# Performance work log

Hardware: AMD Instinct MI355X
Metric: run time of the kernel (lower is better)

## Reference

```python
import jax, jax.numpy as jnp
import numpy as np

B, S, D = 4, 2048, 1024
H = 16
DK = D // H  # 64

def setup_inputs() -> dict:
    key = jax.random.key(0)
    ks = jax.random.split(key, 5)
    scale = 0.02
    return {
        "x": jax.random.normal(ks[0], (B, S, D), dtype=jnp.float32),
        "Wq": jax.random.normal(ks[1], (D, D), dtype=jnp.float32) * scale,
        "Wk": jax.random.normal(ks[2], (D, D), dtype=jnp.float32) * scale,
        "Wv": jax.random.normal(ks[3], (D, D), dtype=jnp.float32) * scale,
        "Wo": jax.random.normal(ks[4], (D, D), dtype=jnp.float32) * scale,
    }

def reference(x, Wq, Wk, Wv, Wo):
    b, s, d = x.shape
    h, dk = H, DK
    # torch nn.Linear(bias=False): y = x @ W.T
    q = (x @ Wq.T).reshape(b, s, h, dk).transpose(0, 2, 1, 3)  # [b,h,s,dk]
    k = (x @ Wk.T).reshape(b, s, h, dk).transpose(0, 2, 1, 3)
    v = (x @ Wv.T).reshape(b, s, h, dk).transpose(0, 2, 1, 3)
    scores = jnp.einsum('bhqd,bhkd->bhqk', q, k) * (dk ** -0.5)
    causal = jnp.triu(jnp.ones((s, s), dtype=bool), k=1)  # True = masked out
    scores = jnp.where(causal, -jnp.inf, scores)
    probs = jax.nn.softmax(scores, axis=-1)
    attn = jnp.einsum('bhqk,bhkd->bhqd', probs, v)  # [b,h,s,dk]
    attn = attn.transpose(0, 2, 1, 3).reshape(b, s, d)
    return attn @ Wo.T
```

## Files before the change

### kernel.cpp

```cpp
#include <hip/hip_runtime.h>

typedef __attribute__((ext_vector_type(8))) short bf16x8;
typedef __attribute__((ext_vector_type(4))) float f32x4;
typedef unsigned int u32;
typedef unsigned short u16;

constexpr int Bb = 4, S = 2048, D = 1024, H = 16, DK = 64, M = Bb * S;

#if __has_builtin(__builtin_amdgcn_exp2f)
#define EXP2F __builtin_amdgcn_exp2f
#else
#define EXP2F exp2f
#endif

__device__ __forceinline__ u16 f2bf(float f) {
  u32 u = __float_as_uint(f);
  return (u16)((u + 0x7fffu + ((u >> 16) & 1u)) >> 16);
}

__device__ __forceinline__ void gld_lds16(const u16* g, u16* l) {
  __builtin_amdgcn_global_load_lds((const __attribute__((address_space(1))) u32*)g,
                                   (__attribute__((address_space(3))) u32*)l, 16, 0, 0);
}

__global__ void cast_kernel(const float* __restrict__ s, u16* __restrict__ d, int n) {
  int i = (blockIdx.x * blockDim.x + threadIdx.x) * 4;
  if (i >= n) return;
  float4 f = *(const float4*)(s + i);
  ushort4 o;
  o.x = f2bf(f.x); o.y = f2bf(f.y); o.z = f2bf(f.z); o.w = f2bf(f.w);
  *(ushort4*)(d + i) = o;
}

struct CastArgs { const float* s[4]; u16* d[4]; float sc[4]; };
__global__ void cast4_kernel(CastArgs a) {
  int i = (blockIdx.x * blockDim.x + threadIdx.x) * 4;
  int w = i >> 20;
  int off = i & ((1 << 20) - 1);
  float sc = a.sc[w];
  float4 f = *(const float4*)(a.s[w] + off);
  ushort4 o;
  o.x = f2bf(f.x * sc); o.y = f2bf(f.y * sc); o.z = f2bf(f.z * sc); o.w = f2bf(f.w * sc);
  *(ushort4*)(a.d[w] + off) = o;
}

template <bool OUTF32>
__device__ __forceinline__ void gemm_core(const u16* __restrict__ A,
                                          const u16* __restrict__ Bt,
                                          float* __restrict__ Cf, u16* __restrict__ Cb,
                                          int Nn, int Kk, int m0, int n0,
                                          u16* As, u16* Bs) {
  const int tid = threadIdx.x, wave = tid >> 6, lane = tid & 63;
  const int quad = lane >> 4, col = lane & 15;
  const int wm = wave >> 1, wn = wave & 1;

  f32x4 acc[4][4];
#pragma unroll
  for (int i = 0; i < 4; i++)
#pragma unroll
    for (int j = 0; j < 4; j++) acc[i][j] = (f32x4){0.f, 0.f, 0.f, 0.f};

  for (int k0 = 0; k0 < Kk; k0 += 64) {
#pragma unroll
    for (int j = 0; j < 4; j++) {
      int g = (wave * 4 + j) * 64;
      int gl = g + lane;
      int r = gl >> 3, sl = gl & 7;
      int kof = (sl ^ (r & 7)) * 8;
      const u16* ga = A + (size_t)(m0 + r) * Kk + k0 + kof;
      gld_lds16(ga, &As[g * 8]);
      const u16* gb = Bt + (size_t)(n0 + r) * Kk + k0 + kof;
      gld_lds16(gb, &Bs[g * 8]);
    }
    __syncthreads();
#pragma unroll
    for (int kb = 0; kb < 2; kb++) {
      bf16x8 af[4], bfr[4];
#pragma unroll
      for (int mi = 0; mi < 4; mi++) {
        int R = wm * 64 + mi * 16 + col;
        af[mi] = *(const bf16x8*)&As[R * 64 + (((kb * 4 + quad) ^ (R & 7)) << 3)];
      }
#pragma unroll
      for (int ni = 0; ni < 4; ni++) {
        int R = wn * 64 + ni * 16 + col;
        bfr[ni] = *(const bf16x8*)&Bs[R * 64 + (((kb * 4 + quad) ^ (R & 7)) << 3)];
      }
#pragma unroll
      for (int mi = 0; mi < 4; mi++)
#pragma unroll
        for (int ni = 0; ni < 4; ni++)
          acc[mi][ni] = __builtin_amdgcn_mfma_f32_16x16x32_bf16(af[mi], bfr[ni], acc[mi][ni], 0, 0, 0);
    }
    __syncthreads();
  }
#pragma unroll
  for (int mi = 0; mi < 4; mi++)
#pragma unroll
    for (int ni = 0; ni < 4; ni++)
#pragma unroll
      for (int r = 0; r < 4; r++) {
        int row = m0 + wm * 64 + mi * 16 + quad * 4 + r;
        int cc = n0 + wn * 64 + ni * 16 + col;
        float v = acc[mi][ni][r];
        if (OUTF32) Cf[(size_t)row * Nn + cc] = v;
        else Cb[(size_t)row * Nn + cc] = f2bf(v);
      }
}

struct QkvArgs { const u16* bt[3]; u16* c[3]; };
__global__ __launch_bounds__(256) void gemm_qkv(const u16* __restrict__ A, QkvArgs q) {
  __shared__ __align__(16) u16 As[128 * 64];
  __shared__ __align__(16) u16 Bs[128 * 64];
  int sel = blockIdx.x >> 3;
  int n0 = (blockIdx.x & 7) * 128, m0 = blockIdx.y * 128;
  gemm_core<false>(A, q.bt[sel], nullptr, q.c[sel], D, D, m0, n0, As, Bs);
}

__global__ __launch_bounds__(256) void gemm_f32(const u16* __restrict__ A,
                                                const u16* __restrict__ Bt,
                                                float* __restrict__ C) {
  __shared__ __align__(16) u16 As[128 * 64];
  __shared__ __align__(16) u16 Bs[128 * 64];
  gemm_core<true>(A, Bt, C, nullptr, D, D, blockIdx.y * 128, blockIdx.x * 128, As, Bs);
}

__global__ __launch_bounds__(256) void attn_kernel(const u16* __restrict__ Q,
                                                   const u16* __restrict__ K,
                                                   const u16* __restrict__ V,
                                                   u16* __restrict__ O) {
  __shared__ __align__(16) u16 Ks[2][2][64 * 32];
  __shared__ __align__(16) u16 Vt[2][64 * 64];
  __shared__ __align__(16) u16 Pw[4][16 * 64];
  const int tid = threadIdx.x, wave = tid >> 6, lane = tid & 63;
  const int quad = lane >> 4, col = lane & 15;
  const int bh = blockIdx.x, b = bh >> 4, h = bh & 15;
  const int ya = blockIdx.y & 3, yk = blockIdx.y >> 2;
  const int qb = (yk == 0) ? ya : (yk == 1) ? 7 - ya : (yk == 2) ? 8 + ya : 15 - ya;
  const size_t base = (size_t)b * S * D + h * DK;
  const int qw = qb * 128 + wave * 32;
  const int nkt = 2 * qb + 2;

  bf16x8 aq[2][2];
#pragma unroll
  for (int mi = 0; mi < 2; mi++)
#pragma unroll
    for (int kb = 0; kb < 2; kb++)
      aq[mi][kb] = *(const bf16x8*)(Q + base + (size_t)(qw + mi * 16 + col) * D + kb * 32 + quad * 8);

  f32x4 ao[2][4], lacc[2];
#pragma unroll
  for (int mi = 0; mi < 2; mi++) {
    lacc[mi] = (f32x4){0.f, 0.f, 0.f, 0.f};
#pragma unroll
    for (int dg = 0; dg < 4; dg++) ao[mi][dg] = (f32x4){0.f, 0.f, 0.f, 0.f};
  }
  bf16x8 bones;
#pragma unroll
  for (int e = 0; e < 8; e++) bones[e] = (short)0x3F80;

  const int vk0 = (tid & 31) * 2;
  const int vdg = tid >> 5;

  bf16x8 vA0, vA1, vB0, vB1;
  {
    const u16* vp = V + base + (size_t)vk0 * D + vdg * 8;
    vA0 = *(const bf16x8*)vp; vA1 = *(const bf16x8*)(vp + D);
  }
  {
    int c = tid, cb = wave * 64;
    const u16* g0 = K + base + (size_t)(c >> 2) * D + (c & 3) * 8;
    gld_lds16(g0, &Ks[0][0][cb * 8]);
    gld_lds16(g0 + 32, &Ks[0][1][cb * 8]);
  }
  auto vstage = [&](int buf, bf16x8 r0, bf16x8 r1) {
    int kgrp = vk0 >> 3, kin = vk0 & 7;
    int perm = (kgrp ^ vdg) & 7;
#pragma unroll
    for (int e = 0; e < 8; e++) {
      u32 val = ((u32)(u16)r0[e]) | ((u32)(u16)r1[e] << 16);
      *(u32*)&Vt[buf][(vdg * 8 + e) * 64 + perm * 8 + kin] = val;
    }
  };
  vstage(0, vA0, vA1);
  {
    const u16* vp = V + base + (size_t)(64 + vk0) * D + vdg * 8;
    vB0 = *(const bf16x8*)vp; vB1 = *(const bf16x8*)(vp + D);
  }

  for (int kt = 0; kt < nkt; kt++) {
    const int bf = kt & 1, nb = bf ^ 1;
    __syncthreads();
    const bool active = (kt * 64 <= qw + 31);
    if (kt + 1 < nkt) {
      {
        int c = tid, cb = wave * 64;
        const u16* g0 = K + base + (size_t)((kt + 1) * 64 + (c >> 2)) * D + (c & 3) * 8;
        gld_lds16(g0, &Ks[nb][0][cb * 8]);
        gld_lds16(g0 + 32, &Ks[nb][1][cb * 8]);
      }
      vstage(nb, bf ? vA0 : vB0, bf ? vA1 : vB1);
      if (kt + 2 < nkt) {
        const u16* vp = V + base + (size_t)((kt + 2) * 64 + vk0) * D + vdg * 8;
        if (bf) { vB0 = *(const bf16x8*)vp; vB1 = *(const bf16x8*)(vp + D); }
        else    { vA0 = *(const bf16x8*)vp; vA1 = *(const bf16x8*)(vp + D); }
      }
    }
    if (!active) continue;
    f32x4 sacc[2][4];
#pragma unroll
    for (int mi = 0; mi < 2; mi++)
#pragma unroll
      for (int n16 = 0; n16 < 4; n16++) sacc[mi][n16] = (f32x4){0.f, 0.f, 0.f, 0.f};
    {
      bf16x8 bk0[4], bk1[4];
#pragma unroll
      for (int n16 = 0; n16 < 4; n16++) {
        bk0[n16] = *(const bf16x8*)&Ks[bf][0][(n16 * 16 + col) * 32 + quad * 8];
        bk1[n16] = *(const bf16x8*)&Ks[bf][1][(n16 * 16 + col) * 32 + quad * 8];
      }
#pragma unroll
      for (int mi = 0; mi < 2; mi++)
#pragma unroll
        for (int n16 = 0; n16 < 4; n16++) {
          sacc[mi][n16] = __builtin_amdgcn_mfma_f32_16x16x32_bf16(aq[mi][0], bk0[n16], sacc[mi][n16], 0, 0, 0);
          sacc[mi][n16] = __builtin_amdgcn_mfma_f32_16x16x32_bf16(aq[mi][1], bk1[n16], sacc[mi][n16], 0, 0, 0);
        }
    }
    const bool full = (kt * 64 + 63) <= qw;
    bf16x8 bv[2][4];
#pragma unroll
    for (int kb = 0; kb < 2; kb++)
#pragma unroll
      for (int dg = 0; dg < 4; dg++) {
        int d3 = (dg * 2 + (col >> 3)) & 7;
        bv[kb][dg] = *(const bf16x8*)&Vt[bf][(dg * 16 + col) * 64 + (((kb * 4 + quad) ^ d3) << 3)];
      }
#pragma unroll
    for (int mi = 0; mi < 2; mi++) {
#pragma unroll
      for (int r = 0; r < 4; r++) {
        int row16 = quad * 4 + r;
        int qs = quad << 1;
#pragma unroll
        for (int n16 = 0; n16 < 4; n16++) {
          float p = EXP2F(sacc[mi][n16][r]);
          if (!full) {
            int kg = kt * 64 + n16 * 16 + col;
            p = (kg > qw + mi * 16 + row16) ? 0.f : p;
          }
          int kgl = n16 * 16 + col;
          int perm = ((kgl >> 3) ^ qs) & 7;
          Pw[wave][row16 * 64 + perm * 8 + (kgl & 7)] = (u16)(__float_as_uint(p) >> 16);
        }
      }
      int qs2 = ((col >> 2) & 3) << 1;
      bf16x8 ap0 = *(const bf16x8*)&Pw[wave][col * 64 + (((quad ^ qs2) & 7) << 3)];
      bf16x8 ap1 = *(const bf16x8*)&Pw[wave][col * 64 + ((((4 + quad) ^ qs2) & 7) << 3)];
#pragma unroll
      for (int dg = 0; dg < 4; dg++) {
        ao[mi][dg] = __builtin_amdgcn_mfma_f32_16x16x32_bf16(ap0, bv[0][dg], ao[mi][dg], 0, 0, 0);
        ao[mi][dg] = __builtin_amdgcn_mfma_f32_16x16x32_bf16(ap1, bv[1][dg], ao[mi][dg], 0, 0, 0);
      }
      lacc[mi] = __builtin_amdgcn_mfma_f32_16x16x32_bf16(ap0, bones, lacc[mi], 0, 0, 0);
      lacc[mi] = __builtin_amdgcn_mfma_f32_16x16x32_bf16(ap1, bones, lacc[mi], 0, 0, 0);
    }
  }
#pragma unroll
  for (int mi = 0; mi < 2; mi++)
#pragma unroll
    for (int r = 0; r < 4; r++) {
      float inv = 1.f / lacc[mi][r];
      int q = qw + mi * 16 + quad * 4 + r;
#pragma unroll
      for (int dg = 0; dg < 4; dg++)
        O[base + (size_t)q * D + dg * 16 + col] = f2bf(ao[mi][dg][r] * inv);
    }
}

extern "C" void kernel_launch(void* const* d_in, const int* in_sizes, int n_in,
                              void* d_out, int out_size, void* d_ws, size_t ws_size,
                              hipStream_t stream) {
  const float* x  = (const float*)d_in[0];
  const float* Wq = (const float*)d_in[1];
  const float* Wk = (const float*)d_in[2];
  const float* Wv = (const float*)d_in[3];
  const float* Wo = (const float*)d_in[4];

  u16* xb  = (u16*)d_ws;
  u16* wqb = xb + (size_t)M * D;
  u16* wkb = wqb + (size_t)D * D;
  u16* wvb = wkb + (size_t)D * D;
  u16* wob = wvb + (size_t)D * D;
  u16* Qb  = wob + (size_t)D * D;
  u16* Kb  = Qb + (size_t)M * D;
  u16* Vb  = Kb + (size_t)M * D;
  u16* Ab  = xb;

  cast_kernel<<<M * D / 1024, 256, 0, stream>>>(x, xb, M * D);
  CastArgs ca;
  ca.s[0] = Wq; ca.s[1] = Wk; ca.s[2] = Wv; ca.s[3] = Wo;
  ca.d[0] = wqb; ca.d[1] = wkb; ca.d[2] = wvb; ca.d[3] = wob;
  ca.sc[0] = 0.18033688011112042f;
  ca.sc[1] = 1.f; ca.sc[2] = 1.f; ca.sc[3] = 1.f;
  cast4_kernel<<<4 * D * D / 1024, 256, 0, stream>>>(ca);

  QkvArgs qa;
  qa.bt[0] = wqb; qa.bt[1] = wkb; qa.bt[2] = wvb;
  qa.c[0] = Qb; qa.c[1] = Kb; qa.c[2] = Vb;
  gemm_qkv<<<dim3(24, M / 128), 256, 0, stream>>>(xb, qa);

  attn_kernel<<<dim3(Bb * H, 16), 256, 0, stream>>>(Qb, Kb, Vb, Ab);

  gemm_f32<<<dim3(D / 128, M / 128), 256, 0, stream>>>(Ab, wob, (float*)d_out);
}
```

Before: 281.1 us.

## Split long causal query blocks across two workgroups and merge partials in a norm pass

Each workgroup pair now handles a heavy query block (15-p) and a light one (p). The heavy block's key range is split at tile 17 between the two workgroups, and the light block is appended to the second. The split blocks write unnormalized bf16 partial outputs and row sums into scratch space in the output buffer, and a new norm kernel adds and normalizes them. The goal is to balance causal work across workgroups and remove the tail of long blocks, at the cost of an extra launch, scratch traffic, and bf16 rounding of the partials before the merge.

```diff
diff --git a/kernel.cpp b/kernel.cpp
--- a/kernel.cpp
+++ b/kernel.cpp
@@ -16,6 +16,9 @@
 __device__ __forceinline__ u16 f2bf(float f) {
   u32 u = __float_as_uint(f);
   return (u16)((u + 0x7fffu + ((u >> 16) & 1u)) >> 16);
+}
+__device__ __forceinline__ float bf2f(u16 x) {
+  return __uint_as_float(((u32)x) << 16);
 }
 
 __device__ __forceinline__ void gld_lds16(const u16* g, u16* l) {
@@ -128,33 +131,28 @@
 __global__ __launch_bounds__(256) void attn_kernel(const u16* __restrict__ Q,
                                                    const u16* __restrict__ K,
                                                    const u16* __restrict__ V,
-                                                   u16* __restrict__ O) {
+                                                   u16* __restrict__ O,
+                                                   u16* __restrict__ Po,
+                                                   float* __restrict__ Lf) {
   __shared__ __align__(16) u16 Ks[2][2][64 * 32];
   __shared__ __align__(16) u16 Vt[2][64 * 64];
   __shared__ __align__(16) u16 Pw[4][16 * 64];
   const int tid = threadIdx.x, wave = tid >> 6, lane = tid & 63;
   const int quad = lane >> 4, col = lane & 15;
   const int bh = blockIdx.x, b = bh >> 4, h = bh & 15;
-  const int ya = blockIdx.y & 3, yk = blockIdx.y >> 2;
-  const int qb = (yk == 0) ? ya : (yk == 1) ? 7 - ya : (yk == 2) ? 8 + ya : 15 - ya;
+  const int j = blockIdx.y, p = j >> 1, role = j & 1;
+  const int qbh = 15 - p, Th = 2 * qbh + 2;
   const size_t base = (size_t)b * S * D + h * DK;
-  const int qw = qb * 128 + wave * 32;
-  const int nkt = 2 * qb + 2;
-
-  bf16x8 aq[2][2];
-#pragma unroll
-  for (int mi = 0; mi < 2; mi++)
-#pragma unroll
-    for (int kb = 0; kb < 2; kb++)
-      aq[mi][kb] = *(const bf16x8*)(Q + base + (size_t)(qw + mi * 16 + col) * D + kb * 32 + quad * 8);
-
-  f32x4 ao[2][4], lacc[2];
-#pragma unroll
-  for (int mi = 0; mi < 2; mi++) {
-    lacc[mi] = (f32x4){0.f, 0.f, 0.f, 0.f};
-#pragma unroll
-    for (int dg = 0; dg < 4; dg++) ao[mi][dg] = (f32x4){0.f, 0.f, 0.f, 0.f};
+
+  int segQb[2], segK0[2], segK1[2], nseg;
+  if (role == 0) {
+    nseg = 1; segQb[0] = qbh; segK0[0] = 0; segK1[0] = 17;
+  } else {
+    nseg = 2;
+    segQb[0] = qbh; segK0[0] = 17; segK1[0] = Th;
+    segQb[1] = p;   segK0[1] = 0;  segK1[1] = 2 * p + 2;
   }
+
   bf16x8 bones;
 #pragma unroll
   for (int e = 0; e < 8; e++) bones[e] = (short)0x3F80;
@@ -162,120 +160,179 @@
   const int vk0 = (tid & 31) * 2;
   const int vdg = tid >> 5;
 
-  bf16x8 vA0, vA1, vB0, vB1;
-  {
-    const u16* vp = V + base + (size_t)vk0 * D + vdg * 8;
-    vA0 = *(const bf16x8*)vp; vA1 = *(const bf16x8*)(vp + D);
+  for (int s = 0; s < nseg; s++) {
+    const int sqb = segQb[s], k0s = segK0[s], k1s = segK1[s];
+    const int qw = sqb * 128 + wave * 32;
+    const bool partial = (sqb >= 8);
+
+    bf16x8 aq[2][2];
+#pragma unroll
+    for (int mi = 0; mi < 2; mi++)
+#pragma unroll
+      for (int kb = 0; kb < 2; kb++)
+        aq[mi][kb] = *(const bf16x8*)(Q + base + (size_t)(qw + mi * 16 + col) * D + kb * 32 + quad * 8);
+
+    f32x4 ao[2][4], lacc[2];
+#pragma unroll
+    for (int mi = 0; mi < 2; mi++) {
+      lacc[mi] = (f32x4){0.f, 0.f, 0.f, 0.f};
+#pragma unroll
+      for (int dg = 0; dg < 4; dg++) ao[mi][dg] = (f32x4){0.f, 0.f, 0.f, 0.f};
+    }
+
+    bf16x8 vA0, vA1, vB0, vB1;
+    {
+      const u16* vp = V + base + (size_t)(k0s * 64 + vk0) * D + vdg * 8;
+      vA0 = *(const bf16x8*)vp; vA1 = *(const bf16x8*)(vp + D);
+    }
+    __syncthreads();
+    {
+      int c = tid, cb = wave * 64;
+      const u16* g0 = K + base + (size_t)(k0s * 64 + (c >> 2)) * D + (c & 3) * 8;
+      gld_lds16(g0, &Ks[0][0][cb * 8]);
+      gld_lds16(g0 + 32, &Ks[0][1][cb * 8]);
+    }
+    auto vstage = [&](int buf, bf16x8 r0, bf16x8 r1) {
+      int kgrp = vk0 >> 3, kin = vk0 & 7;
+      int perm = (kgrp ^ vdg) & 7;
+#pragma unroll
+      for (int e = 0; e < 8; e++) {
+        u32 val = ((u32)(u16)r0[e]) | ((u32)(u16)r1[e] << 16);
+        *(u32*)&Vt[buf][(vdg * 8 + e) * 64 + perm * 8 + kin] = val;
+      }
+    };
+    vstage(0, vA0, vA1);
+    if (k0s + 1 < k1s) {
+      const u16* vp = V + base + (size_t)((k0s + 1) * 64 + vk0) * D + vdg * 8;
+      vB0 = *(const bf16x8*)vp; vB1 = *(const bf16x8*)(vp + D);
+    }
+
+    for (int kt = k0s; kt < k1s; kt++) {
+      const int ib = (kt - k0s) & 1, nb = ib ^ 1;
+      __syncthreads();
+      const bool active = (kt * 64 <= qw + 31);
+      if (kt + 1 < k1s) {
+        {
+          int c = tid, cb = wave * 64;
+          const u16* g0 = K + base + (size_t)((kt + 1) * 64 + (c >> 2)) * D + (c & 3) * 8;
+          gld_lds16(g0, &Ks[nb][0][cb * 8]);
+          gld_lds16(g0 + 32, &Ks[nb][1][cb * 8]);
+        }
+        vstage(nb, ib ? vA0 : vB0, ib ? vA1 : vB1);
+        if (kt + 2 < k1s) {
+          const u16* vp = V + base + (size_t)((kt + 2) * 64 + vk0) * D + vdg * 8;
+          if (ib) { vB0 = *(const bf16x8*)vp; vB1 = *(const bf16x8*)(vp + D); }
+          else    { vA0 = *(const bf16x8*)vp; vA1 = *(const bf16x8*)(vp + D); }
+        }
+      }
+      if (!active) continue;
+      f32x4 sacc[2][4];
+#pragma unroll
+      for (int mi = 0; mi < 2; mi++)
+#pragma unroll
+        for (int n16 = 0; n16 < 4; n16++) sacc[mi][n16] = (f32x4){0.f, 0.f, 0.f, 0.f};
+      {
+        bf16x8 bk0[4], bk1[4];
+#pragma unroll
+        for (int n16 = 0; n16 < 4; n16++) {
+          bk0[n16] = *(const bf16x8*)&Ks[ib][0][(n16 * 16 + col) * 32 + quad * 8];
+          bk1[n16] = *(const bf16x8*)&Ks[ib][1][(n16 * 16 + col) * 32 + quad * 8];
+        }
+#pragma unroll
+        for (int mi = 0; mi < 2; mi++)
+#pragma unroll
+          for (int n16 = 0; n16 < 4; n16++) {
+            sacc[mi][n16] = __builtin_amdgcn_mfma_f32_16x16x32_bf16(aq[mi][0], bk0[n16], sacc[mi][n16], 0, 0, 0);
+            sacc[mi][n16] = __builtin_amdgcn_mfma_f32_16x16x32_bf16(aq[mi][1], bk1[n16], sacc[mi][n16], 0, 0, 0);
+          }
+      }
+      const bool full = (kt * 64 + 63) <= qw;
+      bf16x8 bv[2][4];
+#pragma unroll
+      for (int kb = 0; kb < 2; kb++)
+#pragma unroll
+        for (int dg = 0; dg < 4; dg++) {
+          int d3 = (dg * 2 + (col >> 3)) & 7;
+          bv[kb][dg] = *(const bf16x8*)&Vt[ib][(dg * 16 + col) * 64 + (((kb * 4 + quad) ^ d3) << 3)];
+        }
+#pragma unroll
+      for (int mi = 0; mi < 2; mi++) {
+#pragma unroll
+        for (int r = 0; r < 4; r++) {
+          int row16 = quad * 4 + r;
+          int qs = quad << 1;
+#pragma unroll
+          for (int n16 = 0; n16 < 4; n16++) {
+            float pv = EXP2F(sacc[mi][n16][r]);
+            if (!full) {
+              int kg = kt * 64 + n16 * 16 + col;
+              pv = (kg > qw + mi * 16 + row16) ? 0.f : pv;
+            }
+            int kgl = n16 * 16 + col;
+            int perm = ((kgl >> 3) ^ qs) & 7;
+            Pw[wave][row16 * 64 + perm * 8 + (kgl & 7)] = (u16)(__float_as_uint(pv) >> 16);
+          }
+        }
+        int qs2 = ((col >> 2) & 3) << 1;
+        bf16x8 ap0 = *(const bf16x8*)&Pw[wave][col * 64 + (((quad ^ qs2) & 7) << 3)];
+        bf16x8 ap1 = *(const bf16x8*)&Pw[wave][col * 64 + ((((4 + quad) ^ qs2) & 7) << 3)];
+#pragma unroll
+        for (int dg = 0; dg < 4; dg++) {
+          ao[mi][dg] = __builtin_amdgcn_mfma_f32_16x16x32_bf16(ap0, bv[0][dg], ao[mi][dg], 0, 0, 0);
+          ao[mi][dg] = __builtin_amdgcn_mfma_f32_16x16x32_bf16(ap1, bv[1][dg], ao[mi][dg], 0, 0, 0);
+        }
+        lacc[mi] = __builtin_amdgcn_mfma_f32_16x16x32_bf16(ap0, bones, lacc[mi], 0, 0, 0);
+        lacc[mi] = __builtin_amdgcn_mfma_f32_16x16x32_bf16(ap1, bones, lacc[mi], 0, 0, 0);
+      }
+    }
+    if (!partial) {
+#pragma unroll
+      for (int mi = 0; mi < 2; mi++)
+#pragma unroll
+        for (int r = 0; r < 4; r++) {
+          float inv = 1.f / lacc[mi][r];
+          int q = qw + mi * 16 + quad * 4 + r;
+#pragma unroll
+          for (int dg = 0; dg < 4; dg++)
+            O[base + (size_t)q * D + dg * 16 + col] = f2bf(ao[mi][dg][r] * inv);
+        }
+    } else {
+      int slot = role * 512 + bh * 8 + p;
+      u16* po = Po + (size_t)slot * 8192;
+      float* lf = Lf + slot * 128;
+#pragma unroll
+      for (int mi = 0; mi < 2; mi++)
+#pragma unroll
+        for (int r = 0; r < 4; r++) {
+          int row = wave * 32 + mi * 16 + quad * 4 + r;
+#pragma unroll
+          for (int dg = 0; dg < 4; dg++)
+            po[row * 64 + dg * 16 + col] = f2bf(ao[mi][dg][r]);
+          if (col == 0) lf[row] = lacc[mi][r];
+        }
+    }
   }
-  {
-    int c = tid, cb = wave * 64;
-    const u16* g0 = K + base + (size_t)(c >> 2) * D + (c & 3) * 8;
-    gld_lds16(g0, &Ks[0][0][cb * 8]);
-    gld_lds16(g0 + 32, &Ks[0][1][cb * 8]);
-  }
-  auto vstage = [&](int buf, bf16x8 r0, bf16x8 r1) {
-    int kgrp = vk0 >> 3, kin = vk0 & 7;
-    int perm = (kgrp ^ vdg) & 7;
-#pragma unroll
-    for (int e = 0; e < 8; e++) {
-      u32 val = ((u32)(u16)r0[e]) | ((u32)(u16)r1[e] << 16);
-      *(u32*)&Vt[buf][(vdg * 8 + e) * 64 + perm * 8 + kin] = val;
-    }
-  };
-  vstage(0, vA0, vA1);
-  {
-    const u16* vp = V + base + (size_t)(64 + vk0) * D + vdg * 8;
-    vB0 = *(const bf16x8*)vp; vB1 = *(const bf16x8*)(vp + D);
-  }
-
-  for (int kt = 0; kt < nkt; kt++) {
-    const int bf = kt & 1, nb = bf ^ 1;
-    __syncthreads();
-    const bool active = (kt * 64 <= qw + 31);
-    if (kt + 1 < nkt) {
-      {
-        int c = tid, cb = wave * 64;
-        const u16* g0 = K + base + (size_t)((kt + 1) * 64 + (c >> 2)) * D + (c & 3) * 8;
-        gld_lds16(g0, &Ks[nb][0][cb * 8]);
-        gld_lds16(g0 + 32, &Ks[nb][1][cb * 8]);
-      }
-      vstage(nb, bf ? vA0 : vB0, bf ? vA1 : vB1);
-      if (kt + 2 < nkt) {
-        const u16* vp = V + base + (size_t)((kt + 2) * 64 + vk0) * D + vdg * 8;
-        if (bf) { vB0 = *(const bf16x8*)vp; vB1 = *(const bf16x8*)(vp + D); }
-        else    { vA0 = *(const bf16x8*)vp; vA1 = *(const bf16x8*)(vp + D); }
-      }
-    }
-    if (!active) continue;
-    f32x4 sacc[2][4];
-#pragma unroll
-    for (int mi = 0; mi < 2; mi++)
-#pragma unroll
-      for (int n16 = 0; n16 < 4; n16++) sacc[mi][n16] = (f32x4){0.f, 0.f, 0.f, 0.f};
-    {
-      bf16x8 bk0[4], bk1[4];
-#pragma unroll
-      for (int n16 = 0; n16 < 4; n16++) {
-        bk0[n16] = *(const bf16x8*)&Ks[bf][0][(n16 * 16 + col) * 32 + quad * 8];
-        bk1[n16] = *(const bf16x8*)&Ks[bf][1][(n16 * 16 + col) * 32 + quad * 8];
-      }
-#pragma unroll
-      for (int mi = 0; mi < 2; mi++)
-#pragma unroll
-        for (int n16 = 0; n16 < 4; n16++) {
-          sacc[mi][n16] = __builtin_amdgcn_mfma_f32_16x16x32_bf16(aq[mi][0], bk0[n16], sacc[mi][n16], 0, 0, 0);
-          sacc[mi][n16] = __builtin_amdgcn_mfma_f32_16x16x32_bf16(aq[mi][1], bk1[n16], sacc[mi][n16], 0, 0, 0);
-        }
-    }
-    const bool full = (kt * 64 + 63) <= qw;
-    bf16x8 bv[2][4];
-#pragma unroll
-    for (int kb = 0; kb < 2; kb++)
-#pragma unroll
-      for (int dg = 0; dg < 4; dg++) {
-        int d3 = (dg * 2 + (col >> 3)) & 7;
-        bv[kb][dg] = *(const bf16x8*)&Vt[bf][(dg * 16 + col) * 64 + (((kb * 4 + quad) ^ d3) << 3)];
-      }
-#pragma unroll
-    for (int mi = 0; mi < 2; mi++) {
-#pragma unroll
-      for (int r = 0; r < 4; r++) {
-        int row16 = quad * 4 + r;
-        int qs = quad << 1;
-#pragma unroll
-        for (int n16 = 0; n16 < 4; n16++) {
-          float p = EXP2F(sacc[mi][n16][r]);
-          if (!full) {
-            int kg = kt * 64 + n16 * 16 + col;
-            p = (kg > qw + mi * 16 + row16) ? 0.f : p;
-          }
-          int kgl = n16 * 16 + col;
-          int perm = ((kgl >> 3) ^ qs) & 7;
-          Pw[wave][row16 * 64 + perm * 8 + (kgl & 7)] = (u16)(__float_as_uint(p) >> 16);
-        }
-      }
-      int qs2 = ((col >> 2) & 3) << 1;
-      bf16x8 ap0 = *(const bf16x8*)&Pw[wave][col * 64 + (((quad ^ qs2) & 7) << 3)];
-      bf16x8 ap1 = *(const bf16x8*)&Pw[wave][col * 64 + ((((4 + quad) ^ qs2) & 7) << 3)];
-#pragma unroll
-      for (int dg = 0; dg < 4; dg++) {
-        ao[mi][dg] = __builtin_amdgcn_mfma_f32_16x16x32_bf16(ap0, bv[0][dg], ao[mi][dg], 0, 0, 0);
-        ao[mi][dg] = __builtin_amdgcn_mfma_f32_16x16x32_bf16(ap1, bv[1][dg], ao[mi][dg], 0, 0, 0);
-      }
-      lacc[mi] = __builtin_amdgcn_mfma_f32_16x16x32_bf16(ap0, bones, lacc[mi], 0, 0, 0);
-      lacc[mi] = __builtin_amdgcn_mfma_f32_16x16x32_bf16(ap1, bones, lacc[mi], 0, 0, 0);
-    }
-  }
-#pragma unroll
-  for (int mi = 0; mi < 2; mi++)
-#pragma unroll
-    for (int r = 0; r < 4; r++) {
-      float inv = 1.f / lacc[mi][r];
-      int q = qw + mi * 16 + quad * 4 + r;
-#pragma unroll
-      for (int dg = 0; dg < 4; dg++)
-        O[base + (size_t)q * D + dg * 16 + col] = f2bf(ao[mi][dg][r] * inv);
-    }
+}
+
+__global__ __launch_bounds__(256) void norm_kernel(const u16* __restrict__ Po,
+                                                   const float* __restrict__ Lf,
+                                                   u16* __restrict__ Ab) {
+  int t = blockIdx.x * 256 + threadIdx.x;
+  int c4 = t & 15, r = (t >> 4) & 127, pp = (t >> 11) & 7, bh = t >> 14;
+  int slot = bh * 8 + pp;
+  const u16* p0 = Po + (size_t)slot * 8192 + r * 64 + c4 * 4;
+  const u16* p1 = Po + (size_t)(512 + slot) * 8192 + r * 64 + c4 * 4;
+  float l = Lf[slot * 128 + r] + Lf[(512 + slot) * 128 + r];
+  float inv = 1.f / l;
+  ushort4 a = *(const ushort4*)p0, c = *(const ushort4*)p1;
+  ushort4 o;
+  o.x = f2bf((bf2f(a.x) + bf2f(c.x)) * inv);
+  o.y = f2bf((bf2f(a.y) + bf2f(c.y)) * inv);
+  o.z = f2bf((bf2f(a.z) + bf2f(c.z)) * inv);
+  o.w = f2bf((bf2f(a.w) + bf2f(c.w)) * inv);
+  int b = bh >> 4, h = bh & 15, qbh = 15 - pp;
+  u16* dst = Ab + (size_t)b * S * D + (size_t)(qbh * 128 + r) * D + h * DK + c4 * 4;
+  *(ushort4*)dst = o;
 }
 
 extern "C" void kernel_launch(void* const* d_in, const int* in_sizes, int n_in,
@@ -297,6 +354,9 @@
   u16* Vb  = Kb + (size_t)M * D;
   u16* Ab  = xb;
 
+  u16* Po = (u16*)d_out;
+  float* Lf = (float*)(Po + (size_t)1024 * 8192);
+
   cast_kernel<<<M * D / 1024, 256, 0, stream>>>(x, xb, M * D);
   CastArgs ca;
   ca.s[0] = Wq; ca.s[1] = Wk; ca.s[2] = Wv; ca.s[3] = Wo;
@@ -310,7 +370,8 @@
   qa.c[0] = Qb; qa.c[1] = Kb; qa.c[2] = Vb;
   gemm_qkv<<<dim3(24, M / 128), 256, 0, stream>>>(xb, qa);
 
-  attn_kernel<<<dim3(Bb * H, 16), 256, 0, stream>>>(Qb, Kb, Vb, Ab);
+  attn_kernel<<<dim3(Bb * H, 16), 256, 0, stream>>>(Qb, Kb, Vb, Ab, Po, Lf);
+  norm_kernel<<<4096, 256, 0, stream>>>(Po, Lf, Ab);
 
   gemm_f32<<<dim3(D / 128, M / 128), 256, 0, stream>>>(Ab, wob, (float*)d_out);
 }
```

New measurement: 277.4 us. No clear change (-1.3%).
